# Optimization experiments

Hardware: AMD Instinct MI355X
Metric: run time of the kernel (lower is better)

The kernel has to match this reference:

```python
import jax, jax.numpy as jnp
import numpy as np

D_MODEL = 768
NUM_HEADS = 12
HEAD_DIM = D_MODEL // NUM_HEADS
B, S = 2, 2048


def setup_inputs() -> dict:
    key = jax.random.key(0)
    ks = jax.random.split(key, 12)
    s = 1.0 / np.sqrt(D_MODEL)
    inp = {
        "query": jax.random.normal(ks[0], (B, S, D_MODEL), jnp.float32),
        "key": jax.random.normal(ks[1], (B, S, D_MODEL), jnp.float32),
        "value": jax.random.normal(ks[2], (B, S, D_MODEL), jnp.float32),
        # causal mask; masked_fill(scores, mask == 0, -inf)
        "mask": jnp.tril(jnp.ones((S, S), jnp.int32))[None, None, :, :],
        "Wq": jax.random.uniform(ks[3], (D_MODEL, D_MODEL), jnp.float32, -s, s),
        "bq": jax.random.uniform(ks[4], (D_MODEL,), jnp.float32, -s, s),
        "Wk": jax.random.uniform(ks[5], (D_MODEL, D_MODEL), jnp.float32, -s, s),
        "bk": jax.random.uniform(ks[6], (D_MODEL,), jnp.float32, -s, s),
        "Wv": jax.random.uniform(ks[7], (D_MODEL, D_MODEL), jnp.float32, -s, s),
        "bv": jax.random.uniform(ks[8], (D_MODEL,), jnp.float32, -s, s),
        "Wo": jax.random.uniform(ks[9], (D_MODEL, D_MODEL), jnp.float32, -s, s),
        "bo": jax.random.uniform(ks[10], (D_MODEL,), jnp.float32, -s, s),
    }
    return inp


def reference(query, key, value, mask, Wq, bq, Wk, bk, Wv, bv, Wo, bo):
    Bq, Lq, Dm = query.shape
    Lk = key.shape[1]
    H, Dh = NUM_HEADS, HEAD_DIM
    # projections (torch Linear: x @ W.T + b), split into heads -> [B,H,L,Dh]
    q = (query @ Wq.T + bq).reshape(Bq, Lq, H, Dh).transpose(0, 2, 1, 3)
    k = (key @ Wk.T + bk).reshape(Bq, Lk, H, Dh).transpose(0, 2, 1, 3)
    v = (value @ Wv.T + bv).reshape(Bq, Lk, H, Dh).transpose(0, 2, 1, 3)
    scores = jnp.einsum("bhqd,bhkd->bhqk", q, k) / jnp.sqrt(jnp.float32(Dh))
    scores = jnp.where(mask == 0, -jnp.inf, scores)
    attn = jax.nn.softmax(scores, axis=-1)
    context = jnp.einsum("bhqk,bhkd->bhqd", attn, v)
    context = context.transpose(0, 2, 1, 3).reshape(Bq, Lq, Dm)
    return context @ Wo.T + bo
```

## Files before the change

kernel.cpp:

```cpp
#include <hip/hip_runtime.h>

#define DM    768
#define NH    12
#define NB    2
#define DHD   64
#define SQL   2048
#define MROWS 4096
#define WSZ   589824
#define XSZ   3145728
#define QSCALE 0.18033688f

typedef short  s16x8 __attribute__((ext_vector_type(8)));
typedef float  f32x4 __attribute__((ext_vector_type(4)));
typedef float  f32x16 __attribute__((ext_vector_type(16)));
typedef unsigned short u16x4 __attribute__((ext_vector_type(4)));
typedef unsigned short u16x8 __attribute__((ext_vector_type(8)));
typedef unsigned int   u32x4 __attribute__((ext_vector_type(4)));

static __device__ __forceinline__ unsigned short f2bf(float f) {
    unsigned int u = __builtin_bit_cast(unsigned int, f);
    u += 0x7FFFu + ((u >> 16) & 1u);
    return (unsigned short)(u >> 16);
}

static __device__ __forceinline__ unsigned int cvtpk1(float x, float y) {
    unsigned int r;
    asm("v_cvt_pk_bf16_f32 %0, %1, %2" : "=v"(r) : "v"(x), "v"(y));
    return r;
}

static __device__ __forceinline__ uint2 cvt2(float4 v) {
    return (uint2){cvtpk1(v.x, v.y), cvtpk1(v.z, v.w)};
}

static __device__ __forceinline__ f32x4 mfma16(s16x8 a, s16x8 b, f32x4 c) {
    return __builtin_amdgcn_mfma_f32_16x16x32_bf16(a, b, c, 0, 0, 0);
}
static __device__ __forceinline__ f32x16 mfma32(s16x8 a, s16x8 b, f32x16 c) {
    return __builtin_amdgcn_mfma_f32_32x32x16_bf16(a, b, c, 0, 0, 0);
}

__global__ __launch_bounds__(256)
void prep(const float* __restrict__ Xq, const float* __restrict__ Xk,
          const float* __restrict__ Xv,
          const float* __restrict__ Wq, const float* __restrict__ Wk,
          const float* __restrict__ Wv, const float* __restrict__ Wo,
          unsigned short* __restrict__ Xb, unsigned short* __restrict__ Wb)
{
    const int y = blockIdx.y;
    const float* src;
    unsigned short* dst;
    int nv;
    if (y < 3) {
        src = (y == 0) ? Xq : (y == 1) ? Xk : Xv;
        dst = Xb + (size_t)y * XSZ;
        nv = XSZ / 8;
    } else {
        const int z = y - 3;
        src = (z == 0) ? Wq : (z == 1) ? Wk : (z == 2) ? Wv : Wo;
        dst = Wb + (size_t)z * WSZ;
        nv = WSZ / 8;
    }
    for (int i = blockIdx.x * 256 + threadIdx.x; i < nv; i += gridDim.x * 256) {
        float4 a = *reinterpret_cast<const float4*>(&src[(size_t)i * 8]);
        float4 b = *reinterpret_cast<const float4*>(&src[(size_t)i * 8 + 4]);
        uint2 p0 = cvt2(a), p1 = cvt2(b);
        u32x4 pk = {p0.x, p0.y, p1.x, p1.y};
        *reinterpret_cast<u32x4*>(&dst[(size_t)i * 8]) = pk;
    }
}

__global__ __launch_bounds__(512)
void qkv_proj(const unsigned short* __restrict__ Xb,
              const unsigned short* __restrict__ Wb,
              const float* __restrict__ bq, const float* __restrict__ bk,
              const float* __restrict__ bv,
              unsigned short* __restrict__ Qo, unsigned short* __restrict__ Ko,
              unsigned short* __restrict__ Vo)
{
    const int z = blockIdx.z;
    const unsigned short* X = Xb + (size_t)z * XSZ;
    const unsigned short* W = Wb + (size_t)z * WSZ;
    const float* bias = (z == 0) ? bq : (z == 1) ? bk : bv;
    unsigned short* O = (z == 0) ? Qo : (z == 1) ? Ko : Vo;

    __shared__ unsigned short As[128][72];
    __shared__ unsigned short Bs[128][72];

    const int tid  = threadIdx.x;
    const int lane = tid & 63;
    const int w    = tid >> 6;
    const int wm   = w >> 1, wn = w & 1;
    const int l15  = lane & 15, lg = lane >> 4;
    const int m0   = blockIdx.y * 128;
    const int n0   = blockIdx.x * 128;
    const int ar   = tid >> 2, ac = (tid & 3) << 4;

    f32x4 acc[2][4];
    #pragma unroll
    for (int i = 0; i < 2; ++i)
        #pragma unroll
        for (int j = 0; j < 4; ++j)
            acc[i][j] = (f32x4){0.f, 0.f, 0.f, 0.f};

    u16x8 ra[2], rb[2];
    #pragma unroll
    for (int i = 0; i < 2; ++i) {
        ra[i] = *reinterpret_cast<const u16x8*>(&X[(size_t)(m0 + ar) * DM + ac + i * 8]);
        rb[i] = *reinterpret_cast<const u16x8*>(&W[(size_t)(n0 + ar) * DM + ac + i * 8]);
    }
    #pragma unroll
    for (int i = 0; i < 2; ++i) {
        *reinterpret_cast<u16x8*>(&As[ar][ac + i * 8]) = ra[i];
        *reinterpret_cast<u16x8*>(&Bs[ar][ac + i * 8]) = rb[i];
    }
    __syncthreads();

    for (int k0 = 0; k0 < DM; k0 += 64) {
        const bool more = (k0 + 64 < DM);
        if (more) {
            #pragma unroll
            for (int i = 0; i < 2; ++i) {
                ra[i] = *reinterpret_cast<const u16x8*>(&X[(size_t)(m0 + ar) * DM + k0 + 64 + ac + i * 8]);
                rb[i] = *reinterpret_cast<const u16x8*>(&W[(size_t)(n0 + ar) * DM + k0 + 64 + ac + i * 8]);
            }
        }
        s16x8 af[2][2], bfg[4][2];
        #pragma unroll
        for (int mi = 0; mi < 2; ++mi)
            #pragma unroll
            for (int ks = 0; ks < 2; ++ks)
                af[mi][ks] = *reinterpret_cast<const s16x8*>(&As[wm * 32 + mi * 16 + l15][ks * 32 + lg * 8]);
        #pragma unroll
        for (int nj = 0; nj < 4; ++nj)
            #pragma unroll
            for (int ks = 0; ks < 2; ++ks)
                bfg[nj][ks] = *reinterpret_cast<const s16x8*>(&Bs[wn * 64 + nj * 16 + l15][ks * 32 + lg * 8]);
        #pragma unroll
        for (int mi = 0; mi < 2; ++mi)
            #pragma unroll
            for (int nj = 0; nj < 4; ++nj)
                #pragma unroll
                for (int ks = 0; ks < 2; ++ks)
                    acc[mi][nj] = mfma16(af[mi][ks], bfg[nj][ks], acc[mi][nj]);
        __syncthreads();
        if (more) {
            #pragma unroll
            for (int i = 0; i < 2; ++i) {
                *reinterpret_cast<u16x8*>(&As[ar][ac + i * 8]) = ra[i];
                *reinterpret_cast<u16x8*>(&Bs[ar][ac + i * 8]) = rb[i];
            }
            __syncthreads();
        }
    }

    const float scale = (z == 0) ? QSCALE : 1.0f;
    #pragma unroll
    for (int mi = 0; mi < 2; ++mi) {
        #pragma unroll
        for (int nj = 0; nj < 4; ++nj) {
            int col = n0 + wn * 64 + nj * 16 + l15;
            float bb = bias[col];
            int hh = col >> 6, d = col & 63;
            if (z < 2) {
                #pragma unroll
                for (int r = 0; r < 4; ++r) {
                    int row = m0 + wm * 32 + mi * 16 + (lg << 2) + r;
                    int b = row >> 11, s = row & (SQL - 1);
                    O[(((size_t)(b * NH + hh) * SQL) + s) * DHD + d] =
                        f2bf((acc[mi][nj][r] + bb) * scale);
                }
            } else {
                int row = m0 + wm * 32 + mi * 16 + (lg << 2);
                int b = row >> 11, s = row & (SQL - 1);
                u16x4 pk;
                #pragma unroll
                for (int r = 0; r < 4; ++r) pk[r] = f2bf(acc[mi][nj][r] + bb);
                *reinterpret_cast<u16x4*>(&O[(((size_t)(b * NH + hh) * DHD) + d) * SQL + s]) = pk;
            }
        }
    }
}

__global__ __launch_bounds__(512)
void attn(const unsigned short* __restrict__ Q, const unsigned short* __restrict__ K,
          const unsigned short* __restrict__ Vt, unsigned short* __restrict__ Ctx)
{
    __shared__ float Acc[8][2112];

    const int tid  = threadIdx.x;
    const int lane = tid & 63;
    const int w    = tid >> 6;
    const int hi   = lane >> 5;
    const int l31  = lane & 31;

    const int id  = blockIdx.x;
    const int xcd = id & 7;
    const int rr  = id >> 3;
    const int bh  = xcd * 3 + (rr % 3);
    const int qt  = 63 - rr / 3;
    const int q0  = qt * 32;

    const unsigned short* Qb = Q  + (size_t)bh * SQL * DHD;
    const unsigned short* Kb = K  + (size_t)bh * SQL * DHD;
    const unsigned short* Vb = Vt + (size_t)bh * DHD * SQL;

    s16x8 qf[4];
    #pragma unroll
    for (int t = 0; t < 4; ++t)
        qf[t] = *reinterpret_cast<const s16x8*>(&Qb[(size_t)(q0 + l31) * DHD + t * 16 + hi * 8]);

    f32x16 o0 = {}, o1 = {};
    float m = -__builtin_inff(), l = 0.f;
    const int nkt = (q0 >> 5) + 1;

    int cnt = (w < nkt) ? ((nkt - w + 7) >> 3) : 0;
    int kt  = w;

    while (cnt >= 2) {
        const int ka = kt * 32, kb2 = (kt + 8) * 32;

        s16x8 kfa[4], kfb[4];
        #pragma unroll
        for (int t = 0; t < 4; ++t) {
            kfa[t] = *reinterpret_cast<const s16x8*>(&Kb[(size_t)(ka + l31) * DHD + t * 16 + hi * 8]);
            kfb[t] = *reinterpret_cast<const s16x8*>(&Kb[(size_t)(kb2 + l31) * DHD + t * 16 + hi * 8]);
        }
        s16x8 va00 = *reinterpret_cast<const s16x8*>(&Vb[(size_t)(l31)      * SQL + ka + hi * 8]);
        s16x8 va01 = *reinterpret_cast<const s16x8*>(&Vb[(size_t)(l31)      * SQL + ka + 16 + hi * 8]);
        s16x8 va10 = *reinterpret_cast<const s16x8*>(&Vb[(size_t)(32 + l31) * SQL + ka + hi * 8]);
        s16x8 va11 = *reinterpret_cast<const s16x8*>(&Vb[(size_t)(32 + l31) * SQL + ka + 16 + hi * 8]);
        s16x8 vb00 = *reinterpret_cast<const s16x8*>(&Vb[(size_t)(l31)      * SQL + kb2 + hi * 8]);
        s16x8 vb01 = *reinterpret_cast<const s16x8*>(&Vb[(size_t)(l31)      * SQL + kb2 + 16 + hi * 8]);
        s16x8 vb10 = *reinterpret_cast<const s16x8*>(&Vb[(size_t)(32 + l31) * SQL + kb2 + hi * 8]);
        s16x8 vb11 = *reinterpret_cast<const s16x8*>(&Vb[(size_t)(32 + l31) * SQL + kb2 + 16 + hi * 8]);

        f32x16 sa = {}, sb = {};
        #pragma unroll
        for (int t = 0; t < 4; ++t) sa = mfma32(kfa[t], qf[t], sa);
        #pragma unroll
        for (int t = 0; t < 4; ++t) sb = mfma32(kfb[t], qf[t], sb);

        if (kt + 8 == nkt - 1) {
            #pragma unroll
            for (int r = 0; r < 16; ++r) {
                int kvr = (r & 3) + 8 * (r >> 2) + 4 * hi;
                if (kvr > l31) sb[r] = -1.0e30f;
            }
        }

        float pm = fmaxf(sa[0], sb[0]);
        #pragma unroll
        for (int r = 1; r < 16; ++r) pm = fmaxf(pm, fmaxf(sa[r], sb[r]));
        pm = fmaxf(pm, __shfl_xor(pm, 32));
        const float mn = fmaxf(m, pm);
        const float al = __builtin_amdgcn_exp2f(m - mn);
        m = mn;

        float rs = 0.f;
        #pragma unroll
        for (int r = 0; r < 16; ++r) {
            sa[r] = __builtin_amdgcn_exp2f(sa[r] - mn); rs += sa[r];
            sb[r] = __builtin_amdgcn_exp2f(sb[r] - mn); rs += sb[r];
        }
        rs += __shfl_xor(rs, 32);
        l = l * al + rs;

        #pragma unroll
        for (int r = 0; r < 16; ++r) { o0[r] *= al; o1[r] *= al; }

        s16x8 pfa[2], pfb[2];
        #pragma unroll
        for (int ks = 0; ks < 2; ++ks) {
            const int rb = ks * 8;
            unsigned int a0 = cvtpk1(sa[rb + 0], sa[rb + 1]);
            unsigned int b0 = cvtpk1(sa[rb + 4], sa[rb + 5]);
            asm("v_permlane32_swap_b32 %0, %1" : "+v"(a0), "+v"(b0));
            unsigned int a1 = cvtpk1(sa[rb + 2], sa[rb + 3]);
            unsigned int b1 = cvtpk1(sa[rb + 6], sa[rb + 7]);
            asm("v_permlane32_swap_b32 %0, %1" : "+v"(a1), "+v"(b1));
            u32x4 pw = {a0, a1, b0, b1};
            pfa[ks] = __builtin_bit_cast(s16x8, pw);
        }
        #pragma unroll
        for (int ks = 0; ks < 2; ++ks) {
            const int rb = ks * 8;
            unsigned int a0 = cvtpk1(sb[rb + 0], sb[rb + 1]);
            unsigned int b0 = cvtpk1(sb[rb + 4], sb[rb + 5]);
            asm("v_permlane32_swap_b32 %0, %1" : "+v"(a0), "+v"(b0));
            unsigned int a1 = cvtpk1(sb[rb + 2], sb[rb + 3]);
            unsigned int b1 = cvtpk1(sb[rb + 6], sb[rb + 7]);
            asm("v_permlane32_swap_b32 %0, %1" : "+v"(a1), "+v"(b1));
            u32x4 pw = {a0, a1, b0, b1};
            pfb[ks] = __builtin_bit_cast(s16x8, pw);
        }

        o0 = mfma32(va00, pfa[0], o0);
        o0 = mfma32(va01, pfa[1], o0);
        o1 = mfma32(va10, pfa[0], o1);
        o1 = mfma32(va11, pfa[1], o1);
        o0 = mfma32(vb00, pfb[0], o0);
        o0 = mfma32(vb01, pfb[1], o0);
        o1 = mfma32(vb10, pfb[0], o1);
        o1 = mfma32(vb11, pfb[1], o1);

        kt += 16; cnt -= 2;
    }

    if (cnt) {
        const int ka = kt * 32;
        s16x8 kfa[4];
        #pragma unroll
        for (int t = 0; t < 4; ++t)
            kfa[t] = *reinterpret_cast<const s16x8*>(&Kb[(size_t)(ka + l31) * DHD + t * 16 + hi * 8]);
        s16x8 va00 = *reinterpret_cast<const s16x8*>(&Vb[(size_t)(l31)      * SQL + ka + hi * 8]);
        s16x8 va01 = *reinterpret_cast<const s16x8*>(&Vb[(size_t)(l31)      * SQL + ka + 16 + hi * 8]);
        s16x8 va10 = *reinterpret_cast<const s16x8*>(&Vb[(size_t)(32 + l31) * SQL + ka + hi * 8]);
        s16x8 va11 = *reinterpret_cast<const s16x8*>(&Vb[(size_t)(32 + l31) * SQL + ka + 16 + hi * 8]);

        f32x16 sa = {};
        #pragma unroll
        for (int t = 0; t < 4; ++t) sa = mfma32(kfa[t], qf[t], sa);

        if (kt == nkt - 1) {
            #pragma unroll
            for (int r = 0; r < 16; ++r) {
                int kvr = (r & 3) + 8 * (r >> 2) + 4 * hi;
                if (kvr > l31) sa[r] = -1.0e30f;
            }
        }

        float pm = sa[0];
        #pragma unroll
        for (int r = 1; r < 16; ++r) pm = fmaxf(pm, sa[r]);
        pm = fmaxf(pm, __shfl_xor(pm, 32));
        const float mn = fmaxf(m, pm);
        const float al = __builtin_amdgcn_exp2f(m - mn);
        m = mn;

        float rs = 0.f;
        #pragma unroll
        for (int r = 0; r < 16; ++r) {
            sa[r] = __builtin_amdgcn_exp2f(sa[r] - mn); rs += sa[r];
        }
        rs += __shfl_xor(rs, 32);
        l = l * al + rs;

        #pragma unroll
        for (int r = 0; r < 16; ++r) { o0[r] *= al; o1[r] *= al; }

        s16x8 pfa[2];
        #pragma unroll
        for (int ks = 0; ks < 2; ++ks) {
            const int rb = ks * 8;
            unsigned int a0 = cvtpk1(sa[rb + 0], sa[rb + 1]);
            unsigned int b0 = cvtpk1(sa[rb + 4], sa[rb + 5]);
            asm("v_permlane32_swap_b32 %0, %1" : "+v"(a0), "+v"(b0));
            unsigned int a1 = cvtpk1(sa[rb + 2], sa[rb + 3]);
            unsigned int b1 = cvtpk1(sa[rb + 6], sa[rb + 7]);
            asm("v_permlane32_swap_b32 %0, %1" : "+v"(a1), "+v"(b1));
            u32x4 pw = {a0, a1, b0, b1};
            pfa[ks] = __builtin_bit_cast(s16x8, pw);
        }

        o0 = mfma32(va00, pfa[0], o0);
        o0 = mfma32(va01, pfa[1], o0);
        o1 = mfma32(va10, pfa[0], o1);
        o1 = mfma32(va11, pfa[1], o1);
    }

    #pragma unroll
    for (int r = 0; r < 16; ++r) {
        int d = (r & 3) + 8 * (r >> 2) + 4 * hi;
        Acc[w][d * 32 + l31]        = o0[r];
        Acc[w][(32 + d) * 32 + l31] = o1[r];
    }
    if (hi == 0) { Acc[w][2048 + l31] = m; Acc[w][2080 + l31] = l; }
    __syncthreads();

    {
        const int q  = tid & 31;
        const int d4 = (tid >> 5) << 2;
        float M = -__builtin_inff();
        float mv[8];
        #pragma unroll
        for (int j = 0; j < 8; ++j) { mv[j] = Acc[j][2048 + q]; M = fmaxf(M, mv[j]); }
        float f[8]; float L = 0.f;
        #pragma unroll
        for (int j = 0; j < 8; ++j) {
            f[j] = __builtin_amdgcn_exp2f(mv[j] - M);
            L += f[j] * Acc[j][2080 + q];
        }
        const float invL = 1.0f / L;
        const int b = bh / NH, h = bh % NH;
        u16x4 pk;
        #pragma unroll
        for (int jj = 0; jj < 4; ++jj) {
            int d = d4 + jj;
            float o = 0.f;
            #pragma unroll
            for (int j = 0; j < 8; ++j) o += f[j] * Acc[j][d * 32 + q];
            pk[jj] = f2bf(o * invL);
        }
        *reinterpret_cast<u16x4*>(&Ctx[(((size_t)(b * SQL + q0 + q) * NH) + h) * DHD + d4]) = pk;
    }
}

__global__ __launch_bounds__(256)
void out_proj(const unsigned short* __restrict__ Ctx, const unsigned short* __restrict__ Wob,
              const float* __restrict__ bo, float* __restrict__ Out)
{
    __shared__ unsigned short As[64][72];
    __shared__ unsigned short Bs[64][72];

    const int tid  = threadIdx.x;
    const int lane = tid & 63;
    const int w    = tid >> 6;
    const int wm   = w >> 1, wn = w & 1;
    const int l15  = lane & 15, lg = lane >> 4;
    const int m0   = blockIdx.y * 64;
    const int n0   = blockIdx.x * 64;
    const int ar   = tid >> 2, ac = (tid & 3) << 4;

    f32x4 acc[2][2];
    #pragma unroll
    for (int i = 0; i < 2; ++i)
        #pragma unroll
        for (int j = 0; j < 2; ++j)
            acc[i][j] = (f32x4){0.f, 0.f, 0.f, 0.f};

    u16x8 ra[2], rb[2];
    #pragma unroll
    for (int i = 0; i < 2; ++i) {
        ra[i] = *reinterpret_cast<const u16x8*>(&Ctx[(size_t)(m0 + ar) * DM + ac + i * 8]);
        rb[i] = *reinterpret_cast<const u16x8*>(&Wob[(size_t)(n0 + ar) * DM + ac + i * 8]);
    }
    #pragma unroll
    for (int i = 0; i < 2; ++i) {
        *reinterpret_cast<u16x8*>(&As[ar][ac + i * 8]) = ra[i];
        *reinterpret_cast<u16x8*>(&Bs[ar][ac + i * 8]) = rb[i];
    }
    __syncthreads();

    for (int k0 = 0; k0 < DM; k0 += 64) {
        const bool more = (k0 + 64 < DM);
        if (more) {
            #pragma unroll
            for (int i = 0; i < 2; ++i) {
                ra[i] = *reinterpret_cast<const u16x8*>(&Ctx[(size_t)(m0 + ar) * DM + k0 + 64 + ac + i * 8]);
                rb[i] = *reinterpret_cast<const u16x8*>(&Wob[(size_t)(n0 + ar) * DM + k0 + 64 + ac + i * 8]);
            }
        }
        s16x8 af[2][2], bfg[2][2];
        #pragma unroll
        for (int mi = 0; mi < 2; ++mi)
            #pragma unroll
            for (int ks = 0; ks < 2; ++ks) {
                af[mi][ks]  = *reinterpret_cast<const s16x8*>(&As[wm * 32 + mi * 16 + l15][ks * 32 + lg * 8]);
                bfg[mi][ks] = *reinterpret_cast<const s16x8*>(&Bs[wn * 32 + mi * 16 + l15][ks * 32 + lg * 8]);
            }
        #pragma unroll
        for (int mi = 0; mi < 2; ++mi)
            #pragma unroll
            for (int nj = 0; nj < 2; ++nj)
                #pragma unroll
                for (int ks = 0; ks < 2; ++ks)
                    acc[mi][nj] = mfma16(af[mi][ks], bfg[nj][ks], acc[mi][nj]);
        __syncthreads();
        if (more) {
            #pragma unroll
            for (int i = 0; i < 2; ++i) {
                *reinterpret_cast<u16x8*>(&As[ar][ac + i * 8]) = ra[i];
                *reinterpret_cast<u16x8*>(&Bs[ar][ac + i * 8]) = rb[i];
            }
            __syncthreads();
        }
    }

    #pragma unroll
    for (int mi = 0; mi < 2; ++mi)
        #pragma unroll
        for (int nj = 0; nj < 2; ++nj) {
            int col = n0 + wn * 32 + nj * 16 + l15;
            float bb = bo[col];
            #pragma unroll
            for (int r = 0; r < 4; ++r) {
                int row = m0 + wm * 32 + mi * 16 + (lg << 2) + r;
                Out[(size_t)row * DM + col] = acc[mi][nj][r] + bb;
            }
        }
}

extern "C" void kernel_launch(void* const* d_in, const int* in_sizes, int n_in,
                              void* d_out, int out_size, void* d_ws, size_t ws_size,
                              hipStream_t stream) {
    const float* query = (const float*)d_in[0];
    const float* key   = (const float*)d_in[1];
    const float* value = (const float*)d_in[2];
    const float* Wq = (const float*)d_in[4];
    const float* bq = (const float*)d_in[5];
    const float* Wk = (const float*)d_in[6];
    const float* bk = (const float*)d_in[7];
    const float* Wv = (const float*)d_in[8];
    const float* bv = (const float*)d_in[9];
    const float* Wo = (const float*)d_in[10];
    const float* bo = (const float*)d_in[11];
    float* out = (float*)d_out;

    unsigned short* Wb  = (unsigned short*)d_ws;
    unsigned short* Xb  = Wb  + (size_t)4 * WSZ;
    unsigned short* Qb  = Xb  + (size_t)3 * XSZ;
    unsigned short* Kb  = Qb  + (size_t)XSZ;
    unsigned short* Vtb = Kb  + (size_t)XSZ;
    unsigned short* Ctx = Xb;

    prep<<<dim3(384, 7), 256, 0, stream>>>(query, key, value, Wq, Wk, Wv, Wo, Xb, Wb);
    qkv_proj<<<dim3(6, 32, 3), 512, 0, stream>>>(Xb, Wb, bq, bk, bv, Qb, Kb, Vtb);
    attn<<<dim3(NB * NH * 64), 512, 0, stream>>>(Qb, Kb, Vtb, Ctx);
    out_proj<<<dim3(12, 64), 256, 0, stream>>>(Ctx, Wb + (size_t)3 * WSZ, bo, out);
}
```

Before: 220.5 us.

## Fuse activation bf16 conversion into QKV GEMM, double-buffer LDS, prefetch K, skip rescale

The separate conversion pass over query/key/value is removed. The QKV projection now loads fp32 activations and converts them to bf16 while writing shared memory, so the bf16 intermediate is never written to or read from global memory. The QKV and output GEMMs switch to double-buffered LDS, which removes one barrier per k-step. The attention kernel prefetches the next K tiles one iteration ahead and skips the online-softmax rescale when no lane's max increased. The costs are more register pressure, twice the LDS, and a wave-wide vote per tile.

Measured after the change: 236.3 us. 7.2% more time.

```diff
diff --git a/kernel.cpp b/kernel.cpp
--- a/kernel.cpp
+++ b/kernel.cpp
@@ -41,37 +41,24 @@
 }
 
 __global__ __launch_bounds__(256)
-void prep(const float* __restrict__ Xq, const float* __restrict__ Xk,
-          const float* __restrict__ Xv,
-          const float* __restrict__ Wq, const float* __restrict__ Wk,
-          const float* __restrict__ Wv, const float* __restrict__ Wo,
-          unsigned short* __restrict__ Xb, unsigned short* __restrict__ Wb)
+void prepW(const float* __restrict__ Wq, const float* __restrict__ Wk,
+           const float* __restrict__ Wv, const float* __restrict__ Wo,
+           unsigned short* __restrict__ Wb)
 {
-    const int y = blockIdx.y;
-    const float* src;
-    unsigned short* dst;
-    int nv;
-    if (y < 3) {
-        src = (y == 0) ? Xq : (y == 1) ? Xk : Xv;
-        dst = Xb + (size_t)y * XSZ;
-        nv = XSZ / 8;
-    } else {
-        const int z = y - 3;
-        src = (z == 0) ? Wq : (z == 1) ? Wk : (z == 2) ? Wv : Wo;
-        dst = Wb + (size_t)z * WSZ;
-        nv = WSZ / 8;
-    }
-    for (int i = blockIdx.x * 256 + threadIdx.x; i < nv; i += gridDim.x * 256) {
-        float4 a = *reinterpret_cast<const float4*>(&src[(size_t)i * 8]);
-        float4 b = *reinterpret_cast<const float4*>(&src[(size_t)i * 8 + 4]);
-        uint2 p0 = cvt2(a), p1 = cvt2(b);
-        u32x4 pk = {p0.x, p0.y, p1.x, p1.y};
-        *reinterpret_cast<u32x4*>(&dst[(size_t)i * 8]) = pk;
-    }
+    const int z = blockIdx.y;
+    const float* src = (z == 0) ? Wq : (z == 1) ? Wk : (z == 2) ? Wv : Wo;
+    unsigned short* d = Wb + (size_t)z * WSZ;
+    const int i = blockIdx.x * 256 + threadIdx.x;
+    float4 a = *reinterpret_cast<const float4*>(&src[(size_t)i * 8]);
+    float4 b = *reinterpret_cast<const float4*>(&src[(size_t)i * 8 + 4]);
+    uint2 p0 = cvt2(a), p1 = cvt2(b);
+    u32x4 pk = {p0.x, p0.y, p1.x, p1.y};
+    *reinterpret_cast<u32x4*>(&d[(size_t)i * 8]) = pk;
 }
 
 __global__ __launch_bounds__(512)
-void qkv_proj(const unsigned short* __restrict__ Xb,
+void qkv_proj(const float* __restrict__ Xq, const float* __restrict__ Xk,
+              const float* __restrict__ Xv,
               const unsigned short* __restrict__ Wb,
               const float* __restrict__ bq, const float* __restrict__ bk,
               const float* __restrict__ bv,
@@ -79,13 +66,13 @@
               unsigned short* __restrict__ Vo)
 {
     const int z = blockIdx.z;
-    const unsigned short* X = Xb + (size_t)z * XSZ;
+    const float* X = (z == 0) ? Xq : (z == 1) ? Xk : Xv;
     const unsigned short* W = Wb + (size_t)z * WSZ;
     const float* bias = (z == 0) ? bq : (z == 1) ? bk : bv;
     unsigned short* O = (z == 0) ? Qo : (z == 1) ? Ko : Vo;
 
-    __shared__ unsigned short As[128][72];
-    __shared__ unsigned short Bs[128][72];
+    __shared__ unsigned short As[2][128][72];
+    __shared__ unsigned short Bs[2][128][72];
 
     const int tid  = threadIdx.x;
     const int lane = tid & 63;
@@ -103,39 +90,43 @@
         for (int j = 0; j < 4; ++j)
             acc[i][j] = (f32x4){0.f, 0.f, 0.f, 0.f};
 
-    u16x8 ra[2], rb[2];
-    #pragma unroll
-    for (int i = 0; i < 2; ++i) {
-        ra[i] = *reinterpret_cast<const u16x8*>(&X[(size_t)(m0 + ar) * DM + ac + i * 8]);
+    float4 ra[4]; u16x8 rb[2];
+    #pragma unroll
+    for (int i = 0; i < 4; ++i)
+        ra[i] = *reinterpret_cast<const float4*>(&X[(size_t)(m0 + ar) * DM + ac + i * 4]);
+    #pragma unroll
+    for (int i = 0; i < 2; ++i)
         rb[i] = *reinterpret_cast<const u16x8*>(&W[(size_t)(n0 + ar) * DM + ac + i * 8]);
-    }
-    #pragma unroll
-    for (int i = 0; i < 2; ++i) {
-        *reinterpret_cast<u16x8*>(&As[ar][ac + i * 8]) = ra[i];
-        *reinterpret_cast<u16x8*>(&Bs[ar][ac + i * 8]) = rb[i];
-    }
+    #pragma unroll
+    for (int i = 0; i < 4; ++i)
+        *reinterpret_cast<uint2*>(&As[0][ar][ac + i * 4]) = cvt2(ra[i]);
+    #pragma unroll
+    for (int i = 0; i < 2; ++i)
+        *reinterpret_cast<u16x8*>(&Bs[0][ar][ac + i * 8]) = rb[i];
     __syncthreads();
 
+    int c = 0;
     for (int k0 = 0; k0 < DM; k0 += 64) {
         const bool more = (k0 + 64 < DM);
         if (more) {
             #pragma unroll
-            for (int i = 0; i < 2; ++i) {
-                ra[i] = *reinterpret_cast<const u16x8*>(&X[(size_t)(m0 + ar) * DM + k0 + 64 + ac + i * 8]);
+            for (int i = 0; i < 4; ++i)
+                ra[i] = *reinterpret_cast<const float4*>(&X[(size_t)(m0 + ar) * DM + k0 + 64 + ac + i * 4]);
+            #pragma unroll
+            for (int i = 0; i < 2; ++i)
                 rb[i] = *reinterpret_cast<const u16x8*>(&W[(size_t)(n0 + ar) * DM + k0 + 64 + ac + i * 8]);
-            }
         }
         s16x8 af[2][2], bfg[4][2];
         #pragma unroll
         for (int mi = 0; mi < 2; ++mi)
             #pragma unroll
             for (int ks = 0; ks < 2; ++ks)
-                af[mi][ks] = *reinterpret_cast<const s16x8*>(&As[wm * 32 + mi * 16 + l15][ks * 32 + lg * 8]);
+                af[mi][ks] = *reinterpret_cast<const s16x8*>(&As[c][wm * 32 + mi * 16 + l15][ks * 32 + lg * 8]);
         #pragma unroll
         for (int nj = 0; nj < 4; ++nj)
             #pragma unroll
             for (int ks = 0; ks < 2; ++ks)
-                bfg[nj][ks] = *reinterpret_cast<const s16x8*>(&Bs[wn * 64 + nj * 16 + l15][ks * 32 + lg * 8]);
+                bfg[nj][ks] = *reinterpret_cast<const s16x8*>(&Bs[c][wn * 64 + nj * 16 + l15][ks * 32 + lg * 8]);
         #pragma unroll
         for (int mi = 0; mi < 2; ++mi)
             #pragma unroll
@@ -143,15 +134,16 @@
                 #pragma unroll
                 for (int ks = 0; ks < 2; ++ks)
                     acc[mi][nj] = mfma16(af[mi][ks], bfg[nj][ks], acc[mi][nj]);
+        if (more) {
+            #pragma unroll
+            for (int i = 0; i < 4; ++i)
+                *reinterpret_cast<uint2*>(&As[c ^ 1][ar][ac + i * 4]) = cvt2(ra[i]);
+            #pragma unroll
+            for (int i = 0; i < 2; ++i)
+                *reinterpret_cast<u16x8*>(&Bs[c ^ 1][ar][ac + i * 8]) = rb[i];
+        }
         __syncthreads();
-        if (more) {
-            #pragma unroll
-            for (int i = 0; i < 2; ++i) {
-                *reinterpret_cast<u16x8*>(&As[ar][ac + i * 8]) = ra[i];
-                *reinterpret_cast<u16x8*>(&Bs[ar][ac + i * 8]) = rb[i];
-            }
-            __syncthreads();
-        }
+        c ^= 1;
     }
 
     const float scale = (z == 0) ? QSCALE : 1.0f;
@@ -217,15 +209,24 @@
     int cnt = (w < nkt) ? ((nkt - w + 7) >> 3) : 0;
     int kt  = w;
 
+    s16x8 kA[4], kB[4];
+    if (cnt >= 2) {
+        const int ka = kt * 32, kb2 = (kt + 8) * 32;
+        #pragma unroll
+        for (int t = 0; t < 4; ++t) {
+            kA[t] = *reinterpret_cast<const s16x8*>(&Kb[(size_t)(ka + l31) * DHD + t * 16 + hi * 8]);
+            kB[t] = *reinterpret_cast<const s16x8*>(&Kb[(size_t)(kb2 + l31) * DHD + t * 16 + hi * 8]);
+        }
+    } else if (cnt == 1) {
+        const int ka = kt * 32;
+        #pragma unroll
+        for (int t = 0; t < 4; ++t)
+            kA[t] = *reinterpret_cast<const s16x8*>(&Kb[(size_t)(ka + l31) * DHD + t * 16 + hi * 8]);
+    }
+
     while (cnt >= 2) {
         const int ka = kt * 32, kb2 = (kt + 8) * 32;
 
-        s16x8 kfa[4], kfb[4];
-        #pragma unroll
-        for (int t = 0; t < 4; ++t) {
-            kfa[t] = *reinterpret_cast<const s16x8*>(&Kb[(size_t)(ka + l31) * DHD + t * 16 + hi * 8]);
-            kfb[t] = *reinterpret_cast<const s16x8*>(&Kb[(size_t)(kb2 + l31) * DHD + t * 16 + hi * 8]);
-        }
         s16x8 va00 = *reinterpret_cast<const s16x8*>(&Vb[(size_t)(l31)      * SQL + ka + hi * 8]);
         s16x8 va01 = *reinterpret_cast<const s16x8*>(&Vb[(size_t)(l31)      * SQL + ka + 16 + hi * 8]);
         s16x8 va10 = *reinterpret_cast<const s16x8*>(&Vb[(size_t)(32 + l31) * SQL + ka + hi * 8]);
@@ -237,9 +238,24 @@
 
         f32x16 sa = {}, sb = {};
         #pragma unroll
-        for (int t = 0; t < 4; ++t) sa = mfma32(kfa[t], qf[t], sa);
-        #pragma unroll
-        for (int t = 0; t < 4; ++t) sb = mfma32(kfb[t], qf[t], sb);
+        for (int t = 0; t < 4; ++t) sa = mfma32(kA[t], qf[t], sa);
+        #pragma unroll
+        for (int t = 0; t < 4; ++t) sb = mfma32(kB[t], qf[t], sb);
+
+        const int ncnt = cnt - 2, nkt2 = kt + 16;
+        if (ncnt >= 2) {
+            const int na = nkt2 * 32, nb = (nkt2 + 8) * 32;
+            #pragma unroll
+            for (int t = 0; t < 4; ++t) {
+                kA[t] = *reinterpret_cast<const s16x8*>(&Kb[(size_t)(na + l31) * DHD + t * 16 + hi * 8]);
+                kB[t] = *reinterpret_cast<const s16x8*>(&Kb[(size_t)(nb + l31) * DHD + t * 16 + hi * 8]);
+            }
+        } else if (ncnt == 1) {
+            const int na = nkt2 * 32;
+            #pragma unroll
+            for (int t = 0; t < 4; ++t)
+                kA[t] = *reinterpret_cast<const s16x8*>(&Kb[(size_t)(na + l31) * DHD + t * 16 + hi * 8]);
+        }
 
         if (kt + 8 == nkt - 1) {
             #pragma unroll
@@ -253,21 +269,24 @@
         #pragma unroll
         for (int r = 1; r < 16; ++r) pm = fmaxf(pm, fmaxf(sa[r], sb[r]));
         pm = fmaxf(pm, __shfl_xor(pm, 32));
-        const float mn = fmaxf(m, pm);
-        const float al = __builtin_amdgcn_exp2f(m - mn);
-        m = mn;
+
+        if (!__all(pm <= m)) {
+            const float mn = fmaxf(m, pm);
+            const float al = __builtin_amdgcn_exp2f(m - mn);
+            m = mn;
+            l *= al;
+            #pragma unroll
+            for (int r = 0; r < 16; ++r) { o0[r] *= al; o1[r] *= al; }
+        }
 
         float rs = 0.f;
         #pragma unroll
         for (int r = 0; r < 16; ++r) {
-            sa[r] = __builtin_amdgcn_exp2f(sa[r] - mn); rs += sa[r];
-            sb[r] = __builtin_amdgcn_exp2f(sb[r] - mn); rs += sb[r];
+            sa[r] = __builtin_amdgcn_exp2f(sa[r] - m); rs += sa[r];
+            sb[r] = __builtin_amdgcn_exp2f(sb[r] - m); rs += sb[r];
         }
         rs += __shfl_xor(rs, 32);
-        l = l * al + rs;
-
-        #pragma unroll
-        for (int r = 0; r < 16; ++r) { o0[r] *= al; o1[r] *= al; }
+        l += rs;
 
         s16x8 pfa[2], pfb[2];
         #pragma unroll
@@ -304,15 +323,11 @@
         o1 = mfma32(vb10, pfb[0], o1);
         o1 = mfma32(vb11, pfb[1], o1);
 
-        kt += 16; cnt -= 2;
+        kt = nkt2; cnt = ncnt;
     }
 
     if (cnt) {
         const int ka = kt * 32;
-        s16x8 kfa[4];
-        #pragma unroll
-        for (int t = 0; t < 4; ++t)
-            kfa[t] = *reinterpret_cast<const s16x8*>(&Kb[(size_t)(ka + l31) * DHD + t * 16 + hi * 8]);
         s16x8 va00 = *reinterpret_cast<const s16x8*>(&Vb[(size_t)(l31)      * SQL + ka + hi * 8]);
         s16x8 va01 = *reinterpret_cast<const s16x8*>(&Vb[(size_t)(l31)      * SQL + ka + 16 + hi * 8]);
         s16x8 va10 = *reinterpret_cast<const s16x8*>(&Vb[(size_t)(32 + l31) * SQL + ka + hi * 8]);
@@ -320,7 +335,7 @@
 
         f32x16 sa = {};
         #pragma unroll
-        for (int t = 0; t < 4; ++t) sa = mfma32(kfa[t], qf[t], sa);
+        for (int t = 0; t < 4; ++t) sa = mfma32(kA[t], qf[t], sa);
 
         if (kt == nkt - 1) {
             #pragma unroll
@@ -334,20 +349,23 @@
         #pragma unroll
         for (int r = 1; r < 16; ++r) pm = fmaxf(pm, sa[r]);
         pm = fmaxf(pm, __shfl_xor(pm, 32));
-        const float mn = fmaxf(m, pm);
-        const float al = __builtin_amdgcn_exp2f(m - mn);
-        m = mn;
+
+        if (!__all(pm <= m)) {
+            const float mn = fmaxf(m, pm);
+            const float al = __builtin_amdgcn_exp2f(m - mn);
+            m = mn;
+            l *= al;
+            #pragma unroll
+            for (int r = 0; r < 16; ++r) { o0[r] *= al; o1[r] *= al; }
+        }
 
         float rs = 0.f;
         #pragma unroll
         for (int r = 0; r < 16; ++r) {
-            sa[r] = __builtin_amdgcn_exp2f(sa[r] - mn); rs += sa[r];
+            sa[r] = __builtin_amdgcn_exp2f(sa[r] - m); rs += sa[r];
         }
         rs += __shfl_xor(rs, 32);
-        l = l * al + rs;
-
-        #pragma unroll
-        for (int r = 0; r < 16; ++r) { o0[r] *= al; o1[r] *= al; }
+        l += rs;
 
         s16x8 pfa[2];
         #pragma unroll
@@ -410,8 +428,8 @@
 void out_proj(const unsigned short* __restrict__ Ctx, const unsigned short* __restrict__ Wob,
               const float* __restrict__ bo, float* __restrict__ Out)
 {
-    __shared__ unsigned short As[64][72];
-    __shared__ unsigned short Bs[64][72];
+    __shared__ unsigned short As[2][64][72];
+    __shared__ unsigned short Bs[2][64][72];
 
     const int tid  = threadIdx.x;
     const int lane = tid & 63;
@@ -437,11 +455,12 @@
     }
     #pragma unroll
     for (int i = 0; i < 2; ++i) {
-        *reinterpret_cast<u16x8*>(&As[ar][ac + i * 8]) = ra[i];
-        *reinterpret_cast<u16x8*>(&Bs[ar][ac + i * 8]) = rb[i];
+        *reinterpret_cast<u16x8*>(&As[0][ar][ac + i * 8]) = ra[i];
+        *reinterpret_cast<u16x8*>(&Bs[0][ar][ac + i * 8]) = rb[i];
     }
     __syncthreads();
 
+    int c = 0;
     for (int k0 = 0; k0 < DM; k0 += 64) {
         const bool more = (k0 + 64 < DM);
         if (more) {
@@ -456,8 +475,8 @@
         for (int mi = 0; mi < 2; ++mi)
             #pragma unroll
             for (int ks = 0; ks < 2; ++ks) {
-                af[mi][ks]  = *reinterpret_cast<const s16x8*>(&As[wm * 32 + mi * 16 + l15][ks * 32 + lg * 8]);
-                bfg[mi][ks] = *reinterpret_cast<const s16x8*>(&Bs[wn * 32 + mi * 16 + l15][ks * 32 + lg * 8]);
+                af[mi][ks]  = *reinterpret_cast<const s16x8*>(&As[c][wm * 32 + mi * 16 + l15][ks * 32 + lg * 8]);
+                bfg[mi][ks] = *reinterpret_cast<const s16x8*>(&Bs[c][wn * 32 + mi * 16 + l15][ks * 32 + lg * 8]);
             }
         #pragma unroll
         for (int mi = 0; mi < 2; ++mi)
@@ -466,15 +485,15 @@
                 #pragma unroll
                 for (int ks = 0; ks < 2; ++ks)
                     acc[mi][nj] = mfma16(af[mi][ks], bfg[nj][ks], acc[mi][nj]);
+        if (more) {
+            #pragma unroll
+            for (int i = 0; i < 2; ++i) {
+                *reinterpret_cast<u16x8*>(&As[c ^ 1][ar][ac + i * 8]) = ra[i];
+                *reinterpret_cast<u16x8*>(&Bs[c ^ 1][ar][ac + i * 8]) = rb[i];
+            }
+        }
         __syncthreads();
-        if (more) {
-            #pragma unroll
-            for (int i = 0; i < 2; ++i) {
-                *reinterpret_cast<u16x8*>(&As[ar][ac + i * 8]) = ra[i];
-                *reinterpret_cast<u16x8*>(&Bs[ar][ac + i * 8]) = rb[i];
-            }
-            __syncthreads();
-        }
+        c ^= 1;
     }
 
     #pragma unroll
@@ -508,14 +527,14 @@
     float* out = (float*)d_out;
 
     unsigned short* Wb  = (unsigned short*)d_ws;
-    unsigned short* Xb  = Wb  + (size_t)4 * WSZ;
-    unsigned short* Qb  = Xb  + (size_t)3 * XSZ;
+    unsigned short* Qb  = Wb  + (size_t)4 * WSZ;
     unsigned short* Kb  = Qb  + (size_t)XSZ;
     unsigned short* Vtb = Kb  + (size_t)XSZ;
-    unsigned short* Ctx = Xb;
-
-    prep<<<dim3(384, 7), 256, 0, stream>>>(query, key, value, Wq, Wk, Wv, Wo, Xb, Wb);
-    qkv_proj<<<dim3(6, 32, 3), 512, 0, stream>>>(Xb, Wb, bq, bk, bv, Qb, Kb, Vtb);
+    unsigned short* Ctx = Vtb + (size_t)XSZ;
+
+    prepW<<<dim3(288, 4), 256, 0, stream>>>(Wq, Wk, Wv, Wo, Wb);
+    qkv_proj<<<dim3(6, 32, 3), 512, 0, stream>>>(query, key, value, Wb,
+                                                 bq, bk, bv, Qb, Kb, Vtb);
     attn<<<dim3(NB * NH * 64), 512, 0, stream>>>(Qb, Kb, Vtb, Ctx);
     out_proj<<<dim3(12, 64), 256, 0, stream>>>(Ctx, Wb + (size_t)3 * WSZ, bo, out);
 }
```
